# Kernel tuning notes

Measured on AMD Instinct MI355X. Metric: run time of the kernel, lower is better.

The kernel has to match this reference:

```python
import jax, jax.numpy as jnp
import numpy as np

S_CONST = float(np.log(9.0))   # self.s = log(9)
K = 1.0                        # soft_sign sharpness (config.k)
RHO = 1.0
ALPHA0 = 0.01
BETA0 = 0.1
DECAY = 0.99


def soft_sign(x, k=K):
    # E2Efold soft sign: sigmoid(2*k*x)
    return jax.nn.sigmoid(2.0 * k * x)


def constraint_matrix(x):
    # x: [B, L, 4] -> m: [B, L, L]; pairing constraint AU+CG+UG outer products,
    # symmetrized, with |i-j|<=3 band zeroed (diags mask in torch version).
    base_a, base_u, base_c, base_g = x[..., 0], x[..., 1], x[..., 2], x[..., 3]

    def sym_outer(p, q):
        m = p[:, :, None] * q[:, None, :]
        return m + jnp.swapaxes(m, -1, -2)

    m = sym_outer(base_a, base_u) + sym_outer(base_c, base_g) + sym_outer(base_u, base_g)
    L = x.shape[1]
    i = jnp.arange(L)
    band = jnp.abs(i[:, None] - i[None, :]) <= 3  # [L, L] bool
    return jnp.where(band, jnp.zeros((), m.dtype), m)


def contact_a(a_hat, m):
    a = a_hat * a_hat
    a = (a + jnp.swapaxes(a, -1, -2)) * 0.5
    return a * m


def setup_inputs() -> dict:
    key = jax.random.key(0)
    k1, k2 = jax.random.split(key)
    B, L = 16, 512
    u = jax.random.normal(k1, (B, L, L), jnp.float32) * 2.0
    x = jax.random.uniform(k2, (B, L, 4), jnp.float32)
    return {"u": u, "x": x, "timesteps": 20}


def reference(u, x, timesteps):
    m = constraint_matrix(x)
    u = soft_sign(u - S_CONST) * u
    a_hat = jax.nn.sigmoid(u) * jax.lax.stop_gradient(soft_sign(u - S_CONST))
    a = contact_a(a_hat, m)
    lmbd = jax.lax.stop_gradient(jax.nn.relu(jnp.sum(a, -1) - 1.0))

    # per-step decayed learning rates: step t uses alpha0*decay^t (for grad step)
    # and alpha0*decay^(t+1) for the soft-threshold (torch decays alpha in between)
    t_idx = jnp.arange(timesteps, dtype=jnp.float32)
    alphas = ALPHA0 * DECAY ** t_idx
    betas = BETA0 * DECAY ** t_idx

    def step(carry, ab):
        lmbd, a, a_hat = carry
        alpha, beta = ab
        grad_a = -u / 2.0 + (lmbd * soft_sign(jnp.sum(a, -1) - 1.0))[..., None]
        grad = a_hat * m * (grad_a + jnp.swapaxes(grad_a, -1, -2))
        a_hat_new = a_hat - alpha * grad
        a_hat_new = jax.nn.relu(jnp.abs(a_hat_new) - RHO * alpha * DECAY)
        a_hat_new = jnp.clip(a_hat_new, -1.0, 1.0)
        a_new = contact_a(a_hat_new, m)
        lmbd_new = lmbd + beta * jax.nn.relu(jnp.sum(a_new, -1) - 1.0)
        return (lmbd_new, a_new, a_hat_new), a_new

    _, a_stack = jax.lax.scan(step, (lmbd, a, a_hat), (alphas, betas))
    return a_stack  # [timesteps, B, L, L] == a_t_list[1:]
```

## Files before the change

### kernel.cpp

```cpp
#include <hip/hip_runtime.h>
#include <math.h>

#define BB 16
#define LL 512
#define TS 20
#define TT 64
#define NT (LL / TT)
#define NPAIR (NT * (NT + 1) / 2)
#define NUNIT 32
#define NBLK (BB * NUNIT)
#define BLL (BB * LL * LL)
#define NROW (BB * LL)
#define RSPSTEP (BB * NT * LL)
#define PADI 32

#define S_CONST 2.19722457733621938f

__device__ __forceinline__ float sgm(float v) { return 1.0f / (1.0f + __expf(-v)); }
__device__ __forceinline__ float ahat_of(float up) {
  return sgm(up) * sgm(2.0f * (up - S_CONST));
}

__device__ __forceinline__ void st_agent(float* p, float v) {
  __hip_atomic_store(p, v, __ATOMIC_RELAXED, __HIP_MEMORY_SCOPE_AGENT);
}
__device__ __forceinline__ float ld_agent(const float* p) {
  return __hip_atomic_load(p, __ATOMIC_RELAXED, __HIP_MEMORY_SCOPE_AGENT);
}
__device__ __forceinline__ void bump(int* p) {
  __hip_atomic_fetch_add(p, 1, __ATOMIC_RELAXED, __HIP_MEMORY_SCOPE_AGENT);
}
__device__ __forceinline__ void spin_ge(const int* p, int target) {
  while (__hip_atomic_load(p, __ATOMIC_RELAXED, __HIP_MEMORY_SCOPE_AGENT) < target) {
    __builtin_amdgcn_s_sleep(1);
  }
  asm volatile("" ::: "memory");
}

__device__ __forceinline__ void decode_unit(int p, int& RI, int& RJ, bool& dg) {
  if (p < 28) {
    int base = 0, i = 0;
    while (p >= base + (NT - 1 - i)) { base += NT - 1 - i; ++i; }
    RI = i;
    RJ = i + 1 + (p - base);
    dg = false;
  } else {
    int g = p - 28;
    RI = 2 * g;
    RJ = 2 * g + 1;
    dg = true;
  }
}

__global__ __launch_bounds__(256, 2) void k_fused(const float* __restrict__ u,
                                                  const float* __restrict__ x,
                                                  float* __restrict__ rsp,
                                                  int* __restrict__ arr,
                                                  float* __restrict__ out) {
  __shared__ float t1[TT][TT + 1];
  __shared__ float t2[TT][TT + 1];
  __shared__ float colp1[16][TT];
  __shared__ float colp2[16][TT];
  __shared__ float rp1[TT];
  __shared__ float rp2[TT];
  __shared__ float xr[2][TT][4];
  __shared__ float xt[2][TT][4];
  __shared__ float cI[TT];
  __shared__ float cJ[TT];

  int b = blockIdx.x / NUNIT;
  int p = blockIdx.x % NUNIT;
  int RI, RJ;
  bool dg;
  decode_unit(p, RI, RJ, dg);
  int C1 = dg ? RI : RJ;
  int C2 = dg ? RJ : RI;

  int tid = threadIdx.x;
  int tx = tid & 15, ty = tid >> 4;

  int* ctrI = &arr[(b * NT + RI) * PADI];
  int* ctrJ = &arr[(b * NT + RJ) * PADI];

  if (tid < 128) {
    int which = tid >> 6;
    int r = tid & 63;
    int gi = (which ? RJ : RI) * TT + r;
    const float* xp = x + ((b * LL) + gi) * 4;
    float A = xp[0], U = xp[1], C = xp[2], G = xp[3];
    xr[which][r][0] = A; xr[which][r][1] = U; xr[which][r][2] = C; xr[which][r][3] = G;
    xt[which][r][0] = U; xt[which][r][1] = A + G; xt[which][r][2] = G; xt[which][r][3] = C + U;
  }

  int lrow = 0;
  if (tid < 128) {
    int which = tid >> 6;
    int r = tid & 63;
    lrow = (which ? RJ : RI) * TT + r;
  }
  float lmbd = 0.0f;

  float av1[4][4], av2[4][4];
  float wv1[4][4], wv2[4][4];
  float mv1[4][4], mv2[4][4];

  __syncthreads();

#pragma unroll
  for (int k = 0; k < 4; ++k) {
    int r = ty + 16 * k;
    {
      int i = RI * TT + r;
      int off = (b * LL + i) * LL + C1 * TT + 4 * tx;
      float4 u4 = *reinterpret_cast<const float4*>(u + off);
      float uu[4] = {u4.x, u4.y, u4.z, u4.w};
#pragma unroll
      for (int q = 0; q < 4; ++q) {
        float up = sgm(2.0f * (uu[q] - S_CONST)) * uu[q];
        t1[r][4 * tx + q] = up;
        av1[k][q] = ahat_of(up);
      }
    }
    {
      int i = RJ * TT + r;
      int off = (b * LL + i) * LL + C2 * TT + 4 * tx;
      float4 u4 = *reinterpret_cast<const float4*>(u + off);
      float uu[4] = {u4.x, u4.y, u4.z, u4.w};
#pragma unroll
      for (int q = 0; q < 4; ++q) {
        float up = sgm(2.0f * (uu[q] - S_CONST)) * uu[q];
        t2[r][4 * tx + q] = up;
        av2[k][q] = ahat_of(up);
      }
    }
  }
  __syncthreads();

  {
    float (*T1)[TT + 1] = dg ? t1 : t2;
    float (*T2)[TT + 1] = dg ? t2 : t1;
    float (*xc1)[4] = dg ? xt[0] : xt[1];
    float (*xc2)[4] = dg ? xt[1] : xt[0];
    float* rsp0 = rsp;

#pragma unroll
    for (int k = 0; k < 4; ++k) {
      int r = ty + 16 * k;
      {
        int i = RI * TT + r;
        float rs = 0.0f;
#pragma unroll
        for (int q = 0; q < 4; ++q) {
          int c = 4 * tx + q;
          int j = C1 * TT + c;
          float upT = T1[c][r];
          wv1[k][q] = -0.5f * (t1[r][c] + upT);
          int d = i - j; d = d < 0 ? -d : d;
          float mm = (d <= 3) ? 0.0f
                              : xr[0][r][0] * xc1[c][0] + xr[0][r][1] * xc1[c][1] +
                                    xr[0][r][2] * xc1[c][2] + xr[0][r][3] * xc1[c][3];
          mv1[k][q] = mm;
          float aT = ahat_of(upT);
          float a = av1[k][q];
          rs += 0.5f * (a * a + aT * aT) * mm;
        }
        rs += __shfl_xor(rs, 1); rs += __shfl_xor(rs, 2);
        rs += __shfl_xor(rs, 4); rs += __shfl_xor(rs, 8);
        if (tx == 0) st_agent(&rsp0[(b * NT + C1) * LL + i], rs);
      }
      {
        int i = RJ * TT + r;
        float rs = 0.0f;
#pragma unroll
        for (int q = 0; q < 4; ++q) {
          int c = 4 * tx + q;
          int j = C2 * TT + c;
          float upT = T2[c][r];
          wv2[k][q] = -0.5f * (t2[r][c] + upT);
          int d = i - j; d = d < 0 ? -d : d;
          float mm = (d <= 3) ? 0.0f
                              : xr[1][r][0] * xc2[c][0] + xr[1][r][1] * xc2[c][1] +
                                    xr[1][r][2] * xc2[c][2] + xr[1][r][3] * xc2[c][3];
          mv2[k][q] = mm;
          float aT = ahat_of(upT);
          float a = av2[k][q];
          rs += 0.5f * (a * a + aT * aT) * mm;
        }
        rs += __shfl_xor(rs, 1); rs += __shfl_xor(rs, 2);
        rs += __shfl_xor(rs, 4); rs += __shfl_xor(rs, 8);
        if (tx == 0) st_agent(&rsp0[(b * NT + C2) * LL + i], rs);
      }
    }
  }

  __builtin_amdgcn_s_waitcnt(0);
  __syncthreads();
  if (tid == 0) bump(ctrI);
  if (tid == 64) bump(ctrJ);

  float alpha = 0.01f;
  float beta_prev = 0.0f;

  for (int t = 0; t < TS; ++t) {
    if (tid == 0) spin_ge(ctrI, 8 * (t + 1));
    if (tid == 64) spin_ge(ctrJ, 8 * (t + 1));
    __syncthreads();

    if (tid < 128) {
      const float* rp = rsp + (size_t)t * RSPSTEP + b * NT * LL + lrow;
      float rsv = 0.0f;
#pragma unroll
      for (int ct = 0; ct < NT; ++ct) rsv += ld_agent(rp + ct * LL);
      float dv = rsv - 1.0f;
      float rel = dv > 0.0f ? dv : 0.0f;
      lmbd = (t == 0) ? rel : lmbd + beta_prev * rel;
      float cv = lmbd * sgm(2.0f * dv);
      if (tid >= 64) cJ[tid & 63] = cv; else cI[tid] = cv;
    }
    __syncthreads();

    float thr = alpha * 0.99f;
    float* cc1 = dg ? cI : cJ;
    float* cc2 = dg ? cJ : cI;
    bool last = (t == TS - 1);

    float cp1[4] = {0.f, 0.f, 0.f, 0.f};
    float cp2[4] = {0.f, 0.f, 0.f, 0.f};
#pragma unroll
    for (int k = 0; k < 4; ++k) {
      int r = ty + 16 * k;
      {
        float ci = cI[r];
        float rsv = 0.0f;
#pragma unroll
        for (int q = 0; q < 4; ++q) {
          int c = 4 * tx + q;
          float a = av1[k][q];
          float g = a * mv1[k][q] * (wv1[k][q] + ci + cc1[c]);
          float an = a - alpha * g;
          an = fabsf(an) - thr;
          an = an > 0.0f ? an : 0.0f;
          an = an < 1.0f ? an : 1.0f;
          av1[k][q] = an;
          t1[r][c] = an;
          float v = 0.5f * an * an * mv1[k][q];
          rsv += v;
          cp1[q] += v;
        }
        rsv += __shfl_xor(rsv, 1); rsv += __shfl_xor(rsv, 2);
        rsv += __shfl_xor(rsv, 4); rsv += __shfl_xor(rsv, 8);
        if (tx == 0) rp1[r] = rsv;
      }
      {
        float ci = cJ[r];
        float rsv = 0.0f;
#pragma unroll
        for (int q = 0; q < 4; ++q) {
          int c = 4 * tx + q;
          float a = av2[k][q];
          float g = a * mv2[k][q] * (wv2[k][q] + ci + cc2[c]);
          float an = a - alpha * g;
          an = fabsf(an) - thr;
          an = an > 0.0f ? an : 0.0f;
          an = an < 1.0f ? an : 1.0f;
          av2[k][q] = an;
          t2[r][c] = an;
          float v = 0.5f * an * an * mv2[k][q];
          rsv += v;
          cp2[q] += v;
        }
        rsv += __shfl_xor(rsv, 1); rsv += __shfl_xor(rsv, 2);
        rsv += __shfl_xor(rsv, 4); rsv += __shfl_xor(rsv, 8);
        if (tx == 0) rp2[r] = rsv;
      }
    }
#pragma unroll
    for (int q = 0; q < 4; ++q) {
      colp1[ty][4 * tx + q] = cp1[q];
      colp2[ty][4 * tx + q] = cp2[q];
    }
    __syncthreads();

    if (!last) {
      float* rs_next = rsp + (size_t)(t + 1) * RSPSTEP;
      if (tid < 64) {
        int i = tid;
        float vsum = rp1[i];
        float (*cpA)[TT] = dg ? colp1 : colp2;
#pragma unroll
        for (int y = 0; y < 16; ++y) vsum += cpA[y][i];
        st_agent(&rs_next[(b * NT + C1) * LL + RI * TT + i], vsum);
      } else if (tid < 128) {
        int i = tid - 64;
        float vsum = rp2[i];
        float (*cpB)[TT] = dg ? colp2 : colp1;
#pragma unroll
        for (int y = 0; y < 16; ++y) vsum += cpB[y][i];
        st_agent(&rs_next[(b * NT + C2) * LL + RJ * TT + i], vsum);
      }
      __builtin_amdgcn_s_waitcnt(0);
      __syncthreads();
      if (tid == 0) bump(ctrI);
      if (tid == 64) bump(ctrJ);
    }

    float (*T1)[TT + 1] = dg ? t1 : t2;
    float (*T2)[TT + 1] = dg ? t2 : t1;
    float* op = out + (size_t)t * BLL;
#pragma unroll
    for (int k = 0; k < 4; ++k) {
      int r = ty + 16 * k;
      {
        int i = RI * TT + r;
        int off = (b * LL + i) * LL + C1 * TT + 4 * tx;
        float res[4];
#pragma unroll
        for (int q = 0; q < 4; ++q) {
          int c = 4 * tx + q;
          float a = av1[k][q];
          float bt = T1[c][r];
          res[q] = 0.5f * (a * a + bt * bt) * mv1[k][q];
        }
        *reinterpret_cast<float4*>(op + off) = make_float4(res[0], res[1], res[2], res[3]);
      }
      {
        int i = RJ * TT + r;
        int off = (b * LL + i) * LL + C2 * TT + 4 * tx;
        float res[4];
#pragma unroll
        for (int q = 0; q < 4; ++q) {
          int c = 4 * tx + q;
          float a = av2[k][q];
          float bt = T2[c][r];
          res[q] = 0.5f * (a * a + bt * bt) * mv2[k][q];
        }
        *reinterpret_cast<float4*>(op + off) = make_float4(res[0], res[1], res[2], res[3]);
      }
    }

    beta_prev = (t == 0) ? 0.1f : beta_prev * 0.99f;
    alpha *= 0.99f;
  }
}

__device__ __forceinline__ void decode_pair(int p, int& I, int& J) {
  int base = 0, i = 0;
  while (p >= base + (NT - i)) { base += NT - i; ++i; }
  I = i;
  J = i + (p - base);
}

__global__ __launch_bounds__(256) void k_init(const float* __restrict__ u,
                                              const float* __restrict__ x,
                                              float* __restrict__ w,
                                              float* __restrict__ ah,
                                              float* __restrict__ rowsum) {
  __shared__ float up1[TT][TT + 1];
  __shared__ float up2[TT][TT + 1];
  __shared__ float xr[2][TT][4];
  __shared__ float xt[2][TT][4];

  int b = blockIdx.x / NPAIR;
  int p = blockIdx.x % NPAIR;
  int I, J;
  decode_pair(p, I, J);
  bool diag = (I == J);
  int tid = threadIdx.x;
  int tx = tid & 15, ty = tid >> 4;

  if (tid < 128) {
    int which = tid >> 6;
    int r = tid & 63;
    int gi = (which ? J : I) * TT + r;
    const float* xp = x + ((b * LL) + gi) * 4;
    float A = xp[0], U = xp[1], C = xp[2], G = xp[3];
    xr[which][r][0] = A; xr[which][r][1] = U; xr[which][r][2] = C; xr[which][r][3] = G;
    xt[which][r][0] = U; xt[which][r][1] = A + G; xt[which][r][2] = G; xt[which][r][3] = C + U;
  }

  float a1r[4][4], a2r[4][4];

#pragma unroll
  for (int k = 0; k < 4; ++k) {
    int r = ty + 16 * k;
    {
      int i = I * TT + r;
      int off = (b * LL + i) * LL + J * TT + 4 * tx;
      float4 u4 = *reinterpret_cast<const float4*>(u + off);
      float uu[4] = {u4.x, u4.y, u4.z, u4.w};
      float av[4];
#pragma unroll
      for (int q = 0; q < 4; ++q) {
        float up = sgm(2.0f * (uu[q] - S_CONST)) * uu[q];
        up1[r][4 * tx + q] = up;
        av[q] = ahat_of(up);
        a1r[k][q] = av[q];
      }
      *reinterpret_cast<float4*>(ah + off) = make_float4(av[0], av[1], av[2], av[3]);
    }
    if (!diag) {
      int i = J * TT + r;
      int off = (b * LL + i) * LL + I * TT + 4 * tx;
      float4 u4 = *reinterpret_cast<const float4*>(u + off);
      float uu[4] = {u4.x, u4.y, u4.z, u4.w};
      float av[4];
#pragma unroll
      for (int q = 0; q < 4; ++q) {
        float up = sgm(2.0f * (uu[q] - S_CONST)) * uu[q];
        up2[r][4 * tx + q] = up;
        av[q] = ahat_of(up);
        a2r[k][q] = av[q];
      }
      *reinterpret_cast<float4*>(ah + off) = make_float4(av[0], av[1], av[2], av[3]);
    }
  }
  __syncthreads();

  float (*U2)[TT + 1] = diag ? up1 : up2;

#pragma unroll
  for (int k = 0; k < 4; ++k) {
    int r = ty + 16 * k;
    {
      int i = I * TT + r;
      int off = (b * LL + i) * LL + J * TT + 4 * tx;
      float wv[4];
      float rs = 0.0f;
#pragma unroll
      for (int q = 0; q < 4; ++q) {
        int c = 4 * tx + q;
        int j = J * TT + c;
        float upT = U2[c][r];
        wv[q] = -0.5f * (up1[r][c] + upT);
        int d = i - j; d = d < 0 ? -d : d;
        float mm = (d <= 3) ? 0.0f
                            : xr[0][r][0] * xt[1][c][0] + xr[0][r][1] * xt[1][c][1] +
                                  xr[0][r][2] * xt[1][c][2] + xr[0][r][3] * xt[1][c][3];
        float aT = ahat_of(upT);
        float a = a1r[k][q];
        rs += 0.5f * (a * a + aT * aT) * mm;
      }
      *reinterpret_cast<float4*>(w + off) = make_float4(wv[0], wv[1], wv[2], wv[3]);
      rs += __shfl_xor(rs, 1); rs += __shfl_xor(rs, 2);
      rs += __shfl_xor(rs, 4); rs += __shfl_xor(rs, 8);
      if (tx == 0) atomicAdd(&rowsum[b * LL + i], rs);
    }
    if (!diag) {
      int i = J * TT + r;
      int off = (b * LL + i) * LL + I * TT + 4 * tx;
      float wv[4];
      float rs = 0.0f;
#pragma unroll
      for (int q = 0; q < 4; ++q) {
        int c = 4 * tx + q;
        int j = I * TT + c;
        float upT = up1[c][r];
        wv[q] = -0.5f * (up2[r][c] + upT);
        int d = i - j; d = d < 0 ? -d : d;
        float mm = (d <= 3) ? 0.0f
                            : xr[1][r][0] * xt[0][c][0] + xr[1][r][1] * xt[0][c][1] +
                                  xr[1][r][2] * xt[0][c][2] + xr[1][r][3] * xt[0][c][3];
        float aT = ahat_of(upT);
        float a = a2r[k][q];
        rs += 0.5f * (a * a + aT * aT) * mm;
      }
      *reinterpret_cast<float4*>(w + off) = make_float4(wv[0], wv[1], wv[2], wv[3]);
      rs += __shfl_xor(rs, 1); rs += __shfl_xor(rs, 2);
      rs += __shfl_xor(rs, 4); rs += __shfl_xor(rs, 8);
      if (tx == 0) atomicAdd(&rowsum[b * LL + i], rs);
    }
  }
}

__global__ __launch_bounds__(256) void k_c(float* __restrict__ lmbd,
                                           const float* __restrict__ rs,
                                           float* __restrict__ cc,
                                           float* __restrict__ rsn,
                                           float beta_prev, int first) {
  int idx = blockIdx.x * blockDim.x + threadIdx.x;
  if (idx >= NROW) return;
  float t = rs[idx] - 1.0f;
  float rel = t > 0.0f ? t : 0.0f;
  float l = first ? rel : lmbd[idx] + beta_prev * rel;
  lmbd[idx] = l;
  cc[idx] = l * sgm(2.0f * t);
  rsn[idx] = 0.0f;
}

__global__ __launch_bounds__(256) void k_step(const float* __restrict__ x,
                                              const float* __restrict__ w,
                                              float* __restrict__ ah,
                                              const float* __restrict__ cvec,
                                              float* __restrict__ rsn,
                                              float* __restrict__ out,
                                              float alpha, float thr) {
  __shared__ float an1[TT][TT + 1];
  __shared__ float an2[TT][TT + 1];
  __shared__ float xr[2][TT][4];
  __shared__ float xt[2][TT][4];
  __shared__ float cI[TT];
  __shared__ float cJ[TT];

  int b = blockIdx.x / NPAIR;
  int p = blockIdx.x % NPAIR;
  int I, J;
  decode_pair(p, I, J);
  bool diag = (I == J);
  int tid = threadIdx.x;
  int tx = tid & 15, ty = tid >> 4;

  if (tid < 128) {
    int which = tid >> 6;
    int r = tid & 63;
    int gi = (which ? J : I) * TT + r;
    const float* xp = x + ((b * LL) + gi) * 4;
    float A = xp[0], U = xp[1], C = xp[2], G = xp[3];
    xr[which][r][0] = A; xr[which][r][1] = U; xr[which][r][2] = C; xr[which][r][3] = G;
    xt[which][r][0] = U; xt[which][r][1] = A + G; xt[which][r][2] = G; xt[which][r][3] = C + U;
  } else {
    int t2i = tid - 128;
    int which = t2i >> 6;
    int r = t2i & 63;
    int gi = (which ? J : I) * TT + r;
    float cv = cvec[b * LL + gi];
    if (which) cJ[r] = cv; else cI[r] = cv;
  }
  __syncthreads();

  float m1[4][4], m2[4][4];

#pragma unroll
  for (int k = 0; k < 4; ++k) {
    int r = ty + 16 * k;
    {
      int i = I * TT + r;
      int off = (b * LL + i) * LL + J * TT + 4 * tx;
      float4 a4 = *reinterpret_cast<const float4*>(ah + off);
      float4 w4 = *reinterpret_cast<const float4*>(w + off);
      float av[4] = {a4.x, a4.y, a4.z, a4.w};
      float wv[4] = {w4.x, w4.y, w4.z, w4.w};
      float ci = cI[r];
      float res[4];
#pragma unroll
      for (int q = 0; q < 4; ++q) {
        int c = 4 * tx + q;
        int j = J * TT + c;
        int d = i - j; d = d < 0 ? -d : d;
        float mm = (d <= 3) ? 0.0f
                            : xr[0][r][0] * xt[1][c][0] + xr[0][r][1] * xt[1][c][1] +
                                  xr[0][r][2] * xt[1][c][2] + xr[0][r][3] * xt[1][c][3];
        m1[k][q] = mm;
        float g = av[q] * mm * (wv[q] + ci + cJ[c]);
        float an = av[q] - alpha * g;
        an = fabsf(an) - thr;
        an = an > 0.0f ? an : 0.0f;
        an = an < 1.0f ? an : 1.0f;
        res[q] = an;
        an1[r][c] = an;
      }
      *reinterpret_cast<float4*>(ah + off) = make_float4(res[0], res[1], res[2], res[3]);
    }
    if (!diag) {
      int i = J * TT + r;
      int off = (b * LL + i) * LL + I * TT + 4 * tx;
      float4 a4 = *reinterpret_cast<const float4*>(ah + off);
      float4 w4 = *reinterpret_cast<const float4*>(w + off);
      float av[4] = {a4.x, a4.y, a4.z, a4.w};
      float wv[4] = {w4.x, w4.y, w4.z, w4.w};
      float ci = cJ[r];
      float res[4];
#pragma unroll
      for (int q = 0; q < 4; ++q) {
        int c = 4 * tx + q;
        int j = I * TT + c;
        int d = i - j; d = d < 0 ? -d : d;
        float mm = (d <= 3) ? 0.0f
                            : xr[1][r][0] * xt[0][c][0] + xr[1][r][1] * xt[0][c][1] +
                                  xr[1][r][2] * xt[0][c][2] + xr[1][r][3] * xt[0][c][3];
        m2[k][q] = mm;
        float g = av[q] * mm * (wv[q] + ci + cI[c]);
        float an = av[q] - alpha * g;
        an = fabsf(an) - thr;
        an = an > 0.0f ? an : 0.0f;
        an = an < 1.0f ? an : 1.0f;
        res[q] = an;
        an2[r][c] = an;
      }
      *reinterpret_cast<float4*>(ah + off) = make_float4(res[0], res[1], res[2], res[3]);
    }
  }
  __syncthreads();

  float (*A2)[TT + 1] = diag ? an1 : an2;

#pragma unroll
  for (int k = 0; k < 4; ++k) {
    int r = ty + 16 * k;
    {
      int i = I * TT + r;
      int off = (b * LL + i) * LL + J * TT + 4 * tx;
      float res[4];
      float rs = 0.0f;
#pragma unroll
      for (int q = 0; q < 4; ++q) {
        int c = 4 * tx + q;
        float a = an1[r][c];
        float bt = A2[c][r];
        float v = 0.5f * (a * a + bt * bt) * m1[k][q];
        res[q] = v;
        rs += v;
      }
      *reinterpret_cast<float4*>(out + off) = make_float4(res[0], res[1], res[2], res[3]);
      rs += __shfl_xor(rs, 1); rs += __shfl_xor(rs, 2);
      rs += __shfl_xor(rs, 4); rs += __shfl_xor(rs, 8);
      if (tx == 0) atomicAdd(&rsn[b * LL + i], rs);
    }
    if (!diag) {
      int i = J * TT + r;
      int off = (b * LL + i) * LL + I * TT + 4 * tx;
      float res[4];
      float rs = 0.0f;
#pragma unroll
      for (int q = 0; q < 4; ++q) {
        int c = 4 * tx + q;
        float a = an2[r][c];
        float bt = an1[c][r];
        float v = 0.5f * (a * a + bt * bt) * m2[k][q];
        res[q] = v;
        rs += v;
      }
      *reinterpret_cast<float4*>(out + off) = make_float4(res[0], res[1], res[2], res[3]);
      rs += __shfl_xor(rs, 1); rs += __shfl_xor(rs, 2);
      rs += __shfl_xor(rs, 4); rs += __shfl_xor(rs, 8);
      if (tx == 0) atomicAdd(&rsn[b * LL + i], rs);
    }
  }
}

extern "C" void kernel_launch(void* const* d_in, const int* in_sizes, int n_in,
                              void* d_out, int out_size, void* d_ws, size_t ws_size,
                              hipStream_t stream) {
  const float* u = (const float*)d_in[0];
  const float* x = (const float*)d_in[1];
  float* out = (float*)d_out;
  float* ws = (float*)d_ws;

  float* rsp = ws;
  int* arr = (int*)(ws + (size_t)(TS + 1) * RSPSTEP);
  hipMemsetAsync(arr, 0, BB * NT * PADI * sizeof(int), stream);

  void* args[] = {(void*)&u, (void*)&x, (void*)&rsp, (void*)&arr, (void*)&out};
  hipError_t err = hipLaunchCooperativeKernel((void*)k_fused, dim3(NBLK),
                                              dim3(256), args, 0, stream);
  if (err == hipSuccess) return;

  float* w = ws;
  float* ah = ws + (size_t)BLL;
  float* rsA = ws + 2 * (size_t)BLL;
  float* rsB = rsA + NROW;
  float* cc = rsB + NROW;
  float* lmbd = cc + NROW;

  hipMemsetAsync(rsA, 0, NROW * sizeof(float), stream);

  dim3 grid(BB * NPAIR);
  dim3 block(256);
  k_init<<<grid, block, 0, stream>>>(u, x, w, ah, rsA);

  float* ra = rsA;
  float* rb = rsB;
  for (int t = 0; t < TS; ++t) {
    float alpha = 0.01f * powf(0.99f, (float)t);
    float beta_prev = (t > 0) ? 0.1f * powf(0.99f, (float)(t - 1)) : 0.0f;
    k_c<<<dim3((NROW + 255) / 256), block, 0, stream>>>(lmbd, ra, cc, rb, beta_prev,
                                                        t == 0 ? 1 : 0);
    k_step<<<grid, block, 0, stream>>>(x, w, ah, cc, rb, out + (size_t)t * BLL, alpha,
                                       alpha * 0.99f);
    float* tmp = ra; ra = rb; rb = tmp;
  }
}
```

Measured before the change: 417.9 us.

## Replace counter-based inter-block sync with flag-in-data polling on partial row sums

Removes the per-row-tile atomic counters, the waitcnt+syncthreads+bump after each partial-sum publish, and the spin on counters. Each partial row sum is now stored with +1 offset so a nonzero value signals readiness, and consumers poll each of the eight slots until all are nonzero, subtracting 9 afterwards. This drops a barrier and atomic round trip per step but requires memsetting the whole rsp buffer each launch. It also relies on relaxed stores being visible without explicit fences, and on a value of exactly 0 never being published.

```diff
diff --git a/kernel.cpp b/kernel.cpp
--- a/kernel.cpp
+++ b/kernel.cpp
@@ -12,7 +12,6 @@
 #define BLL (BB * LL * LL)
 #define NROW (BB * LL)
 #define RSPSTEP (BB * NT * LL)
-#define PADI 32
 
 #define S_CONST 2.19722457733621938f
 
@@ -26,15 +25,6 @@
 }
 __device__ __forceinline__ float ld_agent(const float* p) {
   return __hip_atomic_load(p, __ATOMIC_RELAXED, __HIP_MEMORY_SCOPE_AGENT);
-}
-__device__ __forceinline__ void bump(int* p) {
-  __hip_atomic_fetch_add(p, 1, __ATOMIC_RELAXED, __HIP_MEMORY_SCOPE_AGENT);
-}
-__device__ __forceinline__ void spin_ge(const int* p, int target) {
-  while (__hip_atomic_load(p, __ATOMIC_RELAXED, __HIP_MEMORY_SCOPE_AGENT) < target) {
-    __builtin_amdgcn_s_sleep(1);
-  }
-  asm volatile("" ::: "memory");
 }
 
 __device__ __forceinline__ void decode_unit(int p, int& RI, int& RJ, bool& dg) {
@@ -55,7 +45,6 @@
 __global__ __launch_bounds__(256, 2) void k_fused(const float* __restrict__ u,
                                                   const float* __restrict__ x,
                                                   float* __restrict__ rsp,
-                                                  int* __restrict__ arr,
                                                   float* __restrict__ out) {
   __shared__ float t1[TT][TT + 1];
   __shared__ float t2[TT][TT + 1];
@@ -78,9 +67,6 @@
 
   int tid = threadIdx.x;
   int tx = tid & 15, ty = tid >> 4;
-
-  int* ctrI = &arr[(b * NT + RI) * PADI];
-  int* ctrJ = &arr[(b * NT + RJ) * PADI];
 
   if (tid < 128) {
     int which = tid >> 6;
@@ -166,7 +152,7 @@
         }
         rs += __shfl_xor(rs, 1); rs += __shfl_xor(rs, 2);
         rs += __shfl_xor(rs, 4); rs += __shfl_xor(rs, 8);
-        if (tx == 0) st_agent(&rsp0[(b * NT + C1) * LL + i], rs);
+        if (tx == 0) st_agent(&rsp0[(b * NT + C1) * LL + i], rs + 1.0f);
       }
       {
         int i = RJ * TT + r;
@@ -188,30 +174,31 @@
         }
         rs += __shfl_xor(rs, 1); rs += __shfl_xor(rs, 2);
         rs += __shfl_xor(rs, 4); rs += __shfl_xor(rs, 8);
-        if (tx == 0) st_agent(&rsp0[(b * NT + C2) * LL + i], rs);
-      }
-    }
-  }
-
-  __builtin_amdgcn_s_waitcnt(0);
-  __syncthreads();
-  if (tid == 0) bump(ctrI);
-  if (tid == 64) bump(ctrJ);
+        if (tx == 0) st_agent(&rsp0[(b * NT + C2) * LL + i], rs + 1.0f);
+      }
+    }
+  }
 
   float alpha = 0.01f;
   float beta_prev = 0.0f;
 
   for (int t = 0; t < TS; ++t) {
-    if (tid == 0) spin_ge(ctrI, 8 * (t + 1));
-    if (tid == 64) spin_ge(ctrJ, 8 * (t + 1));
-    __syncthreads();
-
     if (tid < 128) {
       const float* rp = rsp + (size_t)t * RSPSTEP + b * NT * LL + lrow;
       float rsv = 0.0f;
-#pragma unroll
-      for (int ct = 0; ct < NT; ++ct) rsv += ld_agent(rp + ct * LL);
-      float dv = rsv - 1.0f;
+      unsigned have = 0u;
+      for (;;) {
+#pragma unroll
+        for (int ct = 0; ct < NT; ++ct) {
+          if (!((have >> ct) & 1u)) {
+            float v = ld_agent(rp + ct * LL);
+            if (v != 0.0f) { rsv += v; have |= (1u << ct); }
+          }
+        }
+        if (have == 0xFFu) break;
+        __builtin_amdgcn_s_sleep(1);
+      }
+      float dv = rsv - 9.0f;
       float rel = dv > 0.0f ? dv : 0.0f;
       lmbd = (t == 0) ? rel : lmbd + beta_prev * rel;
       float cv = lmbd * sgm(2.0f * dv);
@@ -289,19 +276,15 @@
         float (*cpA)[TT] = dg ? colp1 : colp2;
 #pragma unroll
         for (int y = 0; y < 16; ++y) vsum += cpA[y][i];
-        st_agent(&rs_next[(b * NT + C1) * LL + RI * TT + i], vsum);
+        st_agent(&rs_next[(b * NT + C1) * LL + RI * TT + i], vsum + 1.0f);
       } else if (tid < 128) {
         int i = tid - 64;
         float vsum = rp2[i];
         float (*cpB)[TT] = dg ? colp2 : colp1;
 #pragma unroll
         for (int y = 0; y < 16; ++y) vsum += cpB[y][i];
-        st_agent(&rs_next[(b * NT + C2) * LL + RJ * TT + i], vsum);
-      }
-      __builtin_amdgcn_s_waitcnt(0);
-      __syncthreads();
-      if (tid == 0) bump(ctrI);
-      if (tid == 64) bump(ctrJ);
+        st_agent(&rs_next[(b * NT + C2) * LL + RJ * TT + i], vsum + 1.0f);
+      }
     }
 
     float (*T1)[TT + 1] = dg ? t1 : t2;
@@ -646,10 +629,9 @@
   float* ws = (float*)d_ws;
 
   float* rsp = ws;
-  int* arr = (int*)(ws + (size_t)(TS + 1) * RSPSTEP);
-  hipMemsetAsync(arr, 0, BB * NT * PADI * sizeof(int), stream);
-
-  void* args[] = {(void*)&u, (void*)&x, (void*)&rsp, (void*)&arr, (void*)&out};
+  hipMemsetAsync(rsp, 0, (size_t)TS * RSPSTEP * sizeof(float), stream);
+
+  void* args[] = {(void*)&u, (void*)&x, (void*)&rsp, (void*)&out};
   hipError_t err = hipLaunchCooperativeKernel((void*)k_fused, dim3(NBLK),
                                               dim3(256), args, 0, stream);
   if (err == hipSuccess) return;
```

Measured after the change: 441.7 us. +5.7%, slower.
